# Kernel tuning notes

Measured on AMD Instinct MI355X. Metric: run time of the kernel, lower is better.

## Reference

```python
import jax, jax.numpy as jnp
import numpy as np

N_START, N_TO, E, H = 100000, 50000, 1000000, 128

def setup_inputs() -> dict:
    key = jax.random.key(0)
    ks = jax.random.split(key, 8)
    return {
        "z_start": jax.random.normal(ks[0], (N_START, H), dtype=jnp.float32),
        "z_to": jax.random.normal(ks[1], (N_TO, H), dtype=jnp.float32),
        "row": jax.random.randint(ks[2], (E,), 0, N_START, dtype=jnp.int64),
        "col": jax.random.randint(ks[3], (E,), 0, N_TO, dtype=jnp.int64),
        "W1": jax.random.normal(ks[4], (2 * H, H), dtype=jnp.float32) * (1.0 / np.sqrt(2 * H)),
        "b1": jnp.zeros((H,), dtype=jnp.float32),
        "W2": jax.random.normal(ks[5], (H, 1), dtype=jnp.float32) * (1.0 / np.sqrt(H)),
        "b2": jnp.zeros((1,), dtype=jnp.float32),
    }

def reference(z_start, z_to, row, col, W1, b1, W2, b2):
    # gather node embeddings by edge endpoints, concat along feature dim
    z = jnp.concatenate([z_start[row], z_to[col]], axis=-1)  # [E, 2H]
    h = jax.nn.relu(z @ W1 + b1)                              # [E, H]
    out = h @ W2 + b2                                         # [E, 1]
    return out.reshape(-1)
```

## Files before the change

kernel.cpp:

```cpp
#include <hip/hip_runtime.h>
#include <hip/hip_bf16.h>
#include <stdint.h>

typedef unsigned short u16;
typedef unsigned long long u64;
typedef __attribute__((ext_vector_type(8))) short short8;
typedef __attribute__((ext_vector_type(4))) float float4v;
typedef __attribute__((ext_vector_type(2))) _Float16 v2h;

__device__ __forceinline__ u16 f2bf(float x) {
    union { float f; unsigned int u; } v; v.f = x;
    unsigned int r = v.u + 0x7fffu + ((v.u >> 16) & 1u);
    return (u16)(r >> 16);
}

__device__ __forceinline__ v2h mk2h(unsigned int u) {
    union { unsigned int u; v2h h; } c; c.u = u; return c.h;
}

__device__ __forceinline__ float dot2acc(v2h a, v2h b, float s) {
#if __has_builtin(__builtin_amdgcn_fdot2)
    return __builtin_amdgcn_fdot2(a, b, s, false);
#else
    return fmaf((float)a[0], (float)b[0], fmaf((float)a[1], (float)b[1], s));
#endif
}


__global__ __launch_bounds__(256) void w1_pack(
    const float* __restrict__ W1, u16* __restrict__ w1p, int* __restrict__ cursor)
{
    if (blockIdx.x == 0 && threadIdx.x < 8) cursor[threadIdx.x] = 0;
    int w = blockIdx.x * 256 + threadIdx.x;
    int lanep = w & 63, t = (w >> 6) & 7, kc = w >> 9;
    short8 o;
#pragma unroll
    for (int j = 0; j < 8; ++j) {
        int k = kc * 32 + (lanep >> 4) * 8 + j;
        int n = t * 16 + (lanep & 15);
        o[j] = (short)f2bf(W1[k * 128 + n]);
    }
    *(short8*)(w1p + (size_t)w * 8) = o;
}

__global__ __launch_bounds__(256, 3) void uv_gemm(
    const float* __restrict__ zs, const float* __restrict__ zt,
    const u16* __restrict__ w1p, const float* __restrict__ b1,
    char* __restrict__ U8, char* __restrict__ V8,
    float* __restrict__ su, float* __restrict__ sv,
    int M1, int M2, int nU)
{
    const int tid = threadIdx.x, wave = tid >> 6, lane = tid & 63;
    const int m15 = lane & 15, quad = lane >> 4;
    const bool isV = (int)blockIdx.x >= nU;
    const float* zsrc = isV ? zt : zs;
    char* dst = isV ? V8 : U8;
    float* sdst = isV ? sv : su;
    const int row0 = (isV ? ((int)blockIdx.x - nU) : (int)blockIdx.x) * 128;
    const int M = isV ? M2 : M1;
    const int nrows = (M - row0) < 128 ? (M - row0) : 128;
    const char* wsrc = (const char*)(w1p + (isV ? 16384 : 0));

    float4 afl[2][4][2];
#pragma unroll
    for (int mtl = 0; mtl < 2; ++mtl) {
        int r = wave * 32 + mtl * 16 + m15;
        int rr = r < nrows ? r : (nrows - 1);
        const float* rowp = zsrc + (size_t)(row0 + rr) * 128 + quad * 8;
#pragma unroll
        for (int kc = 0; kc < 4; ++kc) {
            afl[mtl][kc][0] = *(const float4*)(rowp + kc * 32);
            afl[mtl][kc][1] = *(const float4*)(rowp + kc * 32 + 4);
        }
    }
    short8 Af[2][4];
#pragma unroll
    for (int mtl = 0; mtl < 2; ++mtl)
#pragma unroll
        for (int kc = 0; kc < 4; ++kc) {
            float4 x = afl[mtl][kc][0], y = afl[mtl][kc][1];
            short8 o;
            o[0] = (short)f2bf(x.x); o[1] = (short)f2bf(x.y);
            o[2] = (short)f2bf(x.z); o[3] = (short)f2bf(x.w);
            o[4] = (short)f2bf(y.x); o[5] = (short)f2bf(y.y);
            o[6] = (short)f2bf(y.z); o[7] = (short)f2bf(y.w);
            Af[mtl][kc] = o;
        }

    float4v acc[2][8];
#pragma unroll
    for (int a = 0; a < 2; ++a)
#pragma unroll
        for (int b = 0; b < 8; ++b)
            acc[a][b] = (float4v){0.f, 0.f, 0.f, 0.f};

#pragma unroll
    for (int kc = 0; kc < 4; ++kc) {
        short8 Bf[8];
#pragma unroll
        for (int t = 0; t < 8; ++t)
            Bf[t] = *(const short8*)(wsrc + ((kc * 8 + t) * 1024 + lane * 16));
#pragma unroll
        for (int t = 0; t < 8; ++t)
#pragma unroll
            for (int mtl = 0; mtl < 2; ++mtl)
                acc[mtl][t] = __builtin_amdgcn_mfma_f32_16x16x32_bf16(
                    Af[mtl][kc], Bf[t], acc[mtl][t], 0, 0, 0);
    }

    float b1v[8];
#pragma unroll
    for (int t = 0; t < 8; ++t) b1v[t] = isV ? 0.f : b1[t * 16 + m15];

#pragma unroll
    for (int mtl = 0; mtl < 2; ++mtl) {
#pragma unroll
        for (int r = 0; r < 4; ++r) {
            const int rr = wave * 32 + mtl * 16 + quad * 4 + r;
            float vals[8];
            float vmax = 0.f;
#pragma unroll
            for (int t = 0; t < 8; ++t) {
                float x = acc[mtl][t][r] + b1v[t];
                vals[t] = x;
                vmax = fmaxf(vmax, fabsf(x));
            }
            vmax = fmaxf(vmax, __shfl_xor(vmax, 1));
            vmax = fmaxf(vmax, __shfl_xor(vmax, 2));
            vmax = fmaxf(vmax, __shfl_xor(vmax, 4));
            vmax = fmaxf(vmax, __shfl_xor(vmax, 8));
            const float scl = vmax * (1.f / 127.f);
            const float rs = vmax > 0.f ? 127.f / vmax : 0.f;
            if (rr < nrows) {
                if (m15 == 0) sdst[row0 + rr] = scl;
                unsigned wlo = 0, whi = 0;
#pragma unroll
                for (int t = 0; t < 4; ++t) {
                    int q = __float2int_rn(vals[t] * rs);
                    q = q > 127 ? 127 : (q < -127 ? -127 : q);
                    wlo |= ((unsigned)q & 255u) << (8 * t);
                }
#pragma unroll
                for (int t = 4; t < 8; ++t) {
                    int q = __float2int_rn(vals[t] * rs);
                    q = q > 127 ? 127 : (q < -127 ? -127 : q);
                    whi |= ((unsigned)q & 255u) << (8 * (t - 4));
                }
                uint2 pk; pk.x = wlo; pk.y = whi;
                *(uint2*)(dst + (size_t)(row0 + rr) * 128 + m15 * 8) = pk;
            }
        }
    }
}

__global__ __launch_bounds__(256) void edge_bin(
    const int* __restrict__ row, const int* __restrict__ col,
    u64* __restrict__ tup, int* __restrict__ cursor,
    int E, float binv, int C,
    const char* __restrict__ U8, const char* __restrict__ V8,
    const float* __restrict__ su, const float* __restrict__ sv,
    const float* __restrict__ W2, const float* __restrict__ b2,
    float* __restrict__ out)
{
    __shared__ int lcnt[8];
    __shared__ int lbase[8];
    const int tid = threadIdx.x;
    if (tid < 8) lcnt[tid] = 0;
    __syncthreads();
    const int eb = blockIdx.x * 4096;
    int rr[16], cc[16], bb[16], rk[16];
#pragma unroll
    for (int it = 0; it < 16; ++it) {
        int e = eb + it * 256 + tid;
        rk[it] = -1;
        if (e < E) {
            int r = row[e], c = col[e];
            int b = (int)((float)r * binv);
            b = b > 7 ? 7 : b;
            rr[it] = r; cc[it] = c; bb[it] = b;
            rk[it] = atomicAdd(&lcnt[b], 1);
        }
    }
    __syncthreads();
    if (tid < 8) lbase[tid] = atomicAdd(&cursor[tid], lcnt[tid]);
    __syncthreads();
#pragma unroll
    for (int it = 0; it < 16; ++it) {
        if (rk[it] < 0) continue;
        int e = eb + it * 256 + tid;
        int slot = lbase[bb[it]] + rk[it];
        if (slot < C) {
            tup[(size_t)bb[it] * C + slot] =
                (u64)(unsigned)rr[it] | ((u64)(unsigned)cc[it] << 17) | ((u64)(unsigned)e << 34);
        } else {
            float a = su[rr[it]], bs = sv[cc[it]];
            const signed char* up = (const signed char*)(U8 + (size_t)rr[it] * 128);
            const signed char* vp = (const signed char*)(V8 + (size_t)cc[it] * 128);
            float s = 0.f;
            for (int p = 0; p < 128; ++p) {
                float h = fmaf(a, (float)up[p], bs * (float)vp[p]);
                h = fmaxf(h, 0.f);
                s = fmaf(h, W2[((p & 7) << 4) + (p >> 3)], s);
            }
            out[e] = s + b2[0];
        }
    }
}

__global__ __launch_bounds__(256) void edge_out(
    const char* __restrict__ U8, const char* __restrict__ V8,
    const float* __restrict__ su, const float* __restrict__ sv,
    const u64* __restrict__ tup, const int* __restrict__ cursor,
    const float* __restrict__ W2, const float* __restrict__ b2,
    float* __restrict__ out, int C, int chunks_per_bin)
{
    const int tid = threadIdx.x, m7 = tid & 7, g = tid >> 3;
    const int bin = (int)blockIdx.x & 7;
    int chunk = (int)blockIdx.x >> 3;
    int cnt = cursor[bin];
    cnt = cnt < C ? cnt : C;

    v2h w2e[4], w2o[4];
#pragma unroll
    for (int w = 0; w < 4; ++w) {
        int c0 = 2 * m7 + (w >> 1);
        int tb = (w & 1) * 4;
        w2e[w] = (v2h){(_Float16)W2[(tb + 0) * 16 + c0], (_Float16)W2[(tb + 2) * 16 + c0]};
        w2o[w] = (v2h){(_Float16)W2[(tb + 1) * 16 + c0], (_Float16)W2[(tb + 3) * 16 + c0]};
    }
    const float b2v = b2[0];
    const v2h zero2 = (v2h){(_Float16)0.f, (_Float16)0.f};
    const _Float16 mh = (_Float16)(-1152.f);
    const v2h m1152 = (v2h){mh, mh};
    const u64* tb8 = tup + (size_t)bin * C;

    for (; chunk * 256 < cnt; chunk += chunks_per_bin) {
        const int base = chunk * 256;

        u64 t[8];
#pragma unroll
        for (int it = 0; it < 8; ++it) {
            int idx = base + it * 32 + g;
            t[it] = tb8[idx < cnt ? idx : cnt - 1];
        }
        __builtin_amdgcn_sched_barrier(0);

        uint4 qu[8], qv[8];
        float fsu[8], fsv[8];
#pragma unroll
        for (int it = 0; it < 8; ++it) {
            int r = (int)(t[it] & 0x1FFFF);
            int c = (int)((t[it] >> 17) & 0x1FFFF);
            qu[it] = *(const uint4*)(U8 + (size_t)(unsigned)r * 128 + m7 * 16);
            qv[it] = *(const uint4*)(V8 + (size_t)(unsigned)c * 128 + m7 * 16);
            fsu[it] = su[r];
            fsv[it] = sv[c];
        }
        __builtin_amdgcn_sched_barrier(0);

#pragma unroll
        for (int it = 0; it < 8; ++it) {
            const float a = fsu[it], b = fsv[it];
            const _Float16 ah = (_Float16)a, bh = (_Float16)b;
            const v2h a2 = (v2h){ah, ah}, bb2 = (v2h){bh, bh};
            const unsigned int* uw = (const unsigned int*)&qu[it];
            const unsigned int* vw = (const unsigned int*)&qv[it];
            float s = 0.f;
#pragma unroll
            for (int w = 0; w < 4; ++w) {
                unsigned int xu = uw[w] ^ 0x80808080u;
                unsigned int xv = vw[w] ^ 0x80808080u;
                v2h due = mk2h((xu & 0x00FF00FFu) | 0x64006400u) + m1152;
                v2h duo = mk2h(((xu >> 8) & 0x00FF00FFu) | 0x64006400u) + m1152;
                v2h dve = mk2h((xv & 0x00FF00FFu) | 0x64006400u) + m1152;
                v2h dvo = mk2h(((xv >> 8) & 0x00FF00FFu) | 0x64006400u) + m1152;
                v2h he = __builtin_elementwise_fma(a2, due, bb2 * dve);
                he = __builtin_elementwise_max(he, zero2);
                s = dot2acc(he, w2e[w], s);
                v2h ho = __builtin_elementwise_fma(a2, duo, bb2 * dvo);
                ho = __builtin_elementwise_max(ho, zero2);
                s = dot2acc(ho, w2o[w], s);
            }
            s += __shfl_xor(s, 1);
            s += __shfl_xor(s, 2);
            s += __shfl_xor(s, 4);
            int idx = base + it * 32 + g;
            if (m7 == 0 && idx < cnt) out[(int)(t[it] >> 34)] = s + b2v;
        }
    }
}

__global__ __launch_bounds__(256) void edge_mlp_naive(
    const float* __restrict__ zs, const float* __restrict__ zt,
    const int* __restrict__ row, const int* __restrict__ col,
    const float* __restrict__ W1, const float* __restrict__ b1,
    const float* __restrict__ W2, const float* __restrict__ b2,
    float* __restrict__ out, int E)
{
    __shared__ float zr[4][256];
    int wave = threadIdx.x >> 6, lane = threadIdx.x & 63;
    int e = blockIdx.x * 4 + wave;
    int ec = e < E ? e : E - 1;
    const float* a = zs + (size_t)row[ec] * 128;
    const float* bb = zt + (size_t)col[ec] * 128;
    zr[wave][lane] = a[lane];
    zr[wave][64 + lane] = a[64 + lane];
    zr[wave][128 + lane] = bb[lane];
    zr[wave][192 + lane] = bb[64 + lane];
    __syncthreads();
    float h0 = b1[lane], h1 = b1[64 + lane];
    for (int k = 0; k < 256; ++k) {
        float zk = zr[wave][k];
        h0 = fmaf(zk, W1[k * 128 + lane], h0);
        h1 = fmaf(zk, W1[k * 128 + 64 + lane], h1);
    }
    h0 = h0 > 0.f ? h0 : 0.f;
    h1 = h1 > 0.f ? h1 : 0.f;
    float s = fmaf(h0, W2[lane], h1 * W2[64 + lane]);
    for (int m = 1; m < 64; m <<= 1) s += __shfl_xor(s, m);
    if (lane == 0 && e < E) out[e] = s + b2[0];
}

extern "C" void kernel_launch(void* const* d_in, const int* in_sizes, int n_in,
                              void* d_out, int out_size, void* d_ws, size_t ws_size,
                              hipStream_t stream) {
    const float* zs = (const float*)d_in[0];
    const float* zt = (const float*)d_in[1];
    const int*  row = (const int*)d_in[2];
    const int*  col = (const int*)d_in[3];
    const float* W1 = (const float*)d_in[4];
    const float* b1 = (const float*)d_in[5];
    const float* W2 = (const float*)d_in[6];
    const float* b2 = (const float*)d_in[7];
    float* out = (float*)d_out;

    const int nzs = in_sizes[0];
    const int nzt = in_sizes[1];
    const int E   = in_sizes[2];
    const int M1  = nzs / 128;
    const int M2  = nzt / 128;

    int C = 65536;
    while (C < E / 4 + 1024) C <<= 1;

    const size_t tup_b = (size_t)8 * C * 8;
    const size_t need = tup_b + 64 + (size_t)M1 * 4 + (size_t)M2 * 4 + 65536
                      + (size_t)nzs + (size_t)nzt;
    const bool shapes_ok = (M1 <= 131072) && (M2 <= 131072) && (E > 0) && (E < (1 << 30));

    if (!shapes_ok || ws_size < need) {
        int nb = (E + 3) / 4;
        edge_mlp_naive<<<nb, 256, 0, stream>>>(zs, zt, row, col, W1, b1, W2, b2, out, E);
        return;
    }

    u64* tup    = (u64*)d_ws;
    int* cursor = (int*)((char*)d_ws + tup_b);
    float* su   = (float*)((char*)cursor + 64);
    float* sv   = su + M1;
    u16* w1p    = (u16*)(sv + M2);
    char* U8    = (char*)(w1p + 32768);
    char* V8    = U8 + (size_t)nzs;

    w1_pack<<<16, 256, 0, stream>>>(W1, w1p, cursor);

    const int nU = (M1 + 127) / 128;
    const int nV = (M2 + 127) / 128;
    uv_gemm<<<nU + nV, 256, 0, stream>>>(zs, zt, w1p, b1, U8, V8, su, sv, M1, M2, nU);

    const int rpb = (M1 + 7) / 8;
    const float binv = 1.0f / (float)rpb;
    edge_bin<<<(E + 4095) / 4096, 256, 0, stream>>>(
        row, col, tup, cursor, E, binv, C, U8, V8, su, sv, W2, b2, out);

    const int cpb = 512;
    edge_out<<<8 * cpb, 256, 0, stream>>>(U8, V8, su, sv, tup, cursor, W2, b2, out, C, cpb);
}
```

Baseline: 179.7 us.

## Merge GEMM and edge binning into one launch, prefetch tuples, use perm decode

The U/V GEMM and edge-binning kernels become one launch whose blocks split by index, so the two phases can overlap and one kernel launch goes away. Because binning no longer waits for the GEMM, the overflow fallback recomputes the full MLP directly from fp32 inputs instead of reading the quantized U/V. The int8 storage switches to an offset-binary uint8 encoding, so edge_out can decode with a single byte-permute against a 0x64 constant instead of XOR, mask and OR. edge_out also returns early for empty chunks and software-prefetches the next chunk's edge tuples while the current one is being computed, which costs extra registers.

```diff
diff --git a/kernel.cpp b/kernel.cpp
--- a/kernel.cpp
+++ b/kernel.cpp
@@ -3,6 +3,7 @@
 #include <stdint.h>
 
 typedef unsigned short u16;
+typedef unsigned char u8;
 typedef unsigned long long u64;
 typedef __attribute__((ext_vector_type(8))) short short8;
 typedef __attribute__((ext_vector_type(4))) float float4v;
@@ -23,6 +24,21 @@
     return __builtin_amdgcn_fdot2(a, b, s, false);
 #else
     return fmaf((float)a[0], (float)b[0], fmaf((float)a[1], (float)b[1], s));
+#endif
+}
+
+__device__ __forceinline__ unsigned perm_even(unsigned x, unsigned k64) {
+#if __has_builtin(__builtin_amdgcn_perm)
+    return __builtin_amdgcn_perm(x, k64, 0x00060004u);
+#else
+    return (x & 0x00FF00FFu) | 0x64006400u;
+#endif
+}
+__device__ __forceinline__ unsigned perm_odd(unsigned x, unsigned k64) {
+#if __has_builtin(__builtin_amdgcn_perm)
+    return __builtin_amdgcn_perm(x, k64, 0x00070005u);
+#else
+    return ((x >> 8) & 0x00FF00FFu) | 0x64006400u;
 #endif
 }
 
@@ -43,172 +59,171 @@
     *(short8*)(w1p + (size_t)w * 8) = o;
 }
 
-__global__ __launch_bounds__(256, 3) void uv_gemm(
+__global__ __launch_bounds__(256, 3) void gemm_bin(
     const float* __restrict__ zs, const float* __restrict__ zt,
     const u16* __restrict__ w1p, const float* __restrict__ b1,
-    char* __restrict__ U8, char* __restrict__ V8,
+    u8* __restrict__ U8, u8* __restrict__ V8,
     float* __restrict__ su, float* __restrict__ sv,
-    int M1, int M2, int nU)
-{
-    const int tid = threadIdx.x, wave = tid >> 6, lane = tid & 63;
-    const int m15 = lane & 15, quad = lane >> 4;
-    const bool isV = (int)blockIdx.x >= nU;
-    const float* zsrc = isV ? zt : zs;
-    char* dst = isV ? V8 : U8;
-    float* sdst = isV ? sv : su;
-    const int row0 = (isV ? ((int)blockIdx.x - nU) : (int)blockIdx.x) * 128;
-    const int M = isV ? M2 : M1;
-    const int nrows = (M - row0) < 128 ? (M - row0) : 128;
-    const char* wsrc = (const char*)(w1p + (isV ? 16384 : 0));
-
-    float4 afl[2][4][2];
-#pragma unroll
-    for (int mtl = 0; mtl < 2; ++mtl) {
-        int r = wave * 32 + mtl * 16 + m15;
-        int rr = r < nrows ? r : (nrows - 1);
-        const float* rowp = zsrc + (size_t)(row0 + rr) * 128 + quad * 8;
-#pragma unroll
-        for (int kc = 0; kc < 4; ++kc) {
-            afl[mtl][kc][0] = *(const float4*)(rowp + kc * 32);
-            afl[mtl][kc][1] = *(const float4*)(rowp + kc * 32 + 4);
-        }
-    }
-    short8 Af[2][4];
-#pragma unroll
-    for (int mtl = 0; mtl < 2; ++mtl)
-#pragma unroll
-        for (int kc = 0; kc < 4; ++kc) {
-            float4 x = afl[mtl][kc][0], y = afl[mtl][kc][1];
-            short8 o;
-            o[0] = (short)f2bf(x.x); o[1] = (short)f2bf(x.y);
-            o[2] = (short)f2bf(x.z); o[3] = (short)f2bf(x.w);
-            o[4] = (short)f2bf(y.x); o[5] = (short)f2bf(y.y);
-            o[6] = (short)f2bf(y.z); o[7] = (short)f2bf(y.w);
-            Af[mtl][kc] = o;
-        }
-
-    float4v acc[2][8];
-#pragma unroll
-    for (int a = 0; a < 2; ++a)
-#pragma unroll
-        for (int b = 0; b < 8; ++b)
-            acc[a][b] = (float4v){0.f, 0.f, 0.f, 0.f};
-
-#pragma unroll
-    for (int kc = 0; kc < 4; ++kc) {
-        short8 Bf[8];
-#pragma unroll
-        for (int t = 0; t < 8; ++t)
-            Bf[t] = *(const short8*)(wsrc + ((kc * 8 + t) * 1024 + lane * 16));
-#pragma unroll
-        for (int t = 0; t < 8; ++t)
-#pragma unroll
-            for (int mtl = 0; mtl < 2; ++mtl)
-                acc[mtl][t] = __builtin_amdgcn_mfma_f32_16x16x32_bf16(
-                    Af[mtl][kc], Bf[t], acc[mtl][t], 0, 0, 0);
-    }
-
-    float b1v[8];
-#pragma unroll
-    for (int t = 0; t < 8; ++t) b1v[t] = isV ? 0.f : b1[t * 16 + m15];
-
-#pragma unroll
-    for (int mtl = 0; mtl < 2; ++mtl) {
-#pragma unroll
-        for (int r = 0; r < 4; ++r) {
-            const int rr = wave * 32 + mtl * 16 + quad * 4 + r;
-            float vals[8];
-            float vmax = 0.f;
-#pragma unroll
-            for (int t = 0; t < 8; ++t) {
-                float x = acc[mtl][t][r] + b1v[t];
-                vals[t] = x;
-                vmax = fmaxf(vmax, fabsf(x));
-            }
-            vmax = fmaxf(vmax, __shfl_xor(vmax, 1));
-            vmax = fmaxf(vmax, __shfl_xor(vmax, 2));
-            vmax = fmaxf(vmax, __shfl_xor(vmax, 4));
-            vmax = fmaxf(vmax, __shfl_xor(vmax, 8));
-            const float scl = vmax * (1.f / 127.f);
-            const float rs = vmax > 0.f ? 127.f / vmax : 0.f;
-            if (rr < nrows) {
-                if (m15 == 0) sdst[row0 + rr] = scl;
-                unsigned wlo = 0, whi = 0;
-#pragma unroll
-                for (int t = 0; t < 4; ++t) {
-                    int q = __float2int_rn(vals[t] * rs);
-                    q = q > 127 ? 127 : (q < -127 ? -127 : q);
-                    wlo |= ((unsigned)q & 255u) << (8 * t);
-                }
-#pragma unroll
-                for (int t = 4; t < 8; ++t) {
-                    int q = __float2int_rn(vals[t] * rs);
-                    q = q > 127 ? 127 : (q < -127 ? -127 : q);
-                    whi |= ((unsigned)q & 255u) << (8 * (t - 4));
-                }
-                uint2 pk; pk.x = wlo; pk.y = whi;
-                *(uint2*)(dst + (size_t)(row0 + rr) * 128 + m15 * 8) = pk;
-            }
-        }
-    }
-}
-
-__global__ __launch_bounds__(256) void edge_bin(
+    int M1, int M2, int nU, int nGemm,
     const int* __restrict__ row, const int* __restrict__ col,
     u64* __restrict__ tup, int* __restrict__ cursor,
     int E, float binv, int C,
-    const char* __restrict__ U8, const char* __restrict__ V8,
-    const float* __restrict__ su, const float* __restrict__ sv,
-    const float* __restrict__ W2, const float* __restrict__ b2,
-    float* __restrict__ out)
+    const float* __restrict__ W1, const float* __restrict__ W2,
+    const float* __restrict__ b2, float* __restrict__ out)
 {
     __shared__ int lcnt[8];
     __shared__ int lbase[8];
-    const int tid = threadIdx.x;
-    if (tid < 8) lcnt[tid] = 0;
-    __syncthreads();
-    const int eb = blockIdx.x * 4096;
-    int rr[16], cc[16], bb[16], rk[16];
-#pragma unroll
-    for (int it = 0; it < 16; ++it) {
-        int e = eb + it * 256 + tid;
-        rk[it] = -1;
-        if (e < E) {
-            int r = row[e], c = col[e];
-            int b = (int)((float)r * binv);
-            b = b > 7 ? 7 : b;
-            rr[it] = r; cc[it] = c; bb[it] = b;
-            rk[it] = atomicAdd(&lcnt[b], 1);
-        }
-    }
-    __syncthreads();
-    if (tid < 8) lbase[tid] = atomicAdd(&cursor[tid], lcnt[tid]);
-    __syncthreads();
-#pragma unroll
-    for (int it = 0; it < 16; ++it) {
-        if (rk[it] < 0) continue;
-        int e = eb + it * 256 + tid;
-        int slot = lbase[bb[it]] + rk[it];
-        if (slot < C) {
-            tup[(size_t)bb[it] * C + slot] =
-                (u64)(unsigned)rr[it] | ((u64)(unsigned)cc[it] << 17) | ((u64)(unsigned)e << 34);
-        } else {
-            float a = su[rr[it]], bs = sv[cc[it]];
-            const signed char* up = (const signed char*)(U8 + (size_t)rr[it] * 128);
-            const signed char* vp = (const signed char*)(V8 + (size_t)cc[it] * 128);
-            float s = 0.f;
-            for (int p = 0; p < 128; ++p) {
-                float h = fmaf(a, (float)up[p], bs * (float)vp[p]);
-                h = fmaxf(h, 0.f);
-                s = fmaf(h, W2[((p & 7) << 4) + (p >> 3)], s);
-            }
-            out[e] = s + b2[0];
+
+    if ((int)blockIdx.x < nGemm) {
+        const int tid = threadIdx.x, wave = tid >> 6, lane = tid & 63;
+        const int m15 = lane & 15, quad = lane >> 4;
+        const bool isV = (int)blockIdx.x >= nU;
+        const float* zsrc = isV ? zt : zs;
+        u8* dst = isV ? V8 : U8;
+        float* sdst = isV ? sv : su;
+        const int row0 = (isV ? ((int)blockIdx.x - nU) : (int)blockIdx.x) * 128;
+        const int M = isV ? M2 : M1;
+        const int nrows = (M - row0) < 128 ? (M - row0) : 128;
+        const char* wsrc = (const char*)(w1p + (isV ? 16384 : 0));
+
+        float4 afl[2][4][2];
+#pragma unroll
+        for (int mtl = 0; mtl < 2; ++mtl) {
+            int r = wave * 32 + mtl * 16 + m15;
+            int rr = r < nrows ? r : (nrows - 1);
+            const float* rowp = zsrc + (size_t)(row0 + rr) * 128 + quad * 8;
+#pragma unroll
+            for (int kc = 0; kc < 4; ++kc) {
+                afl[mtl][kc][0] = *(const float4*)(rowp + kc * 32);
+                afl[mtl][kc][1] = *(const float4*)(rowp + kc * 32 + 4);
+            }
+        }
+        short8 Af[2][4];
+#pragma unroll
+        for (int mtl = 0; mtl < 2; ++mtl)
+#pragma unroll
+            for (int kc = 0; kc < 4; ++kc) {
+                float4 x = afl[mtl][kc][0], y = afl[mtl][kc][1];
+                short8 o;
+                o[0] = (short)f2bf(x.x); o[1] = (short)f2bf(x.y);
+                o[2] = (short)f2bf(x.z); o[3] = (short)f2bf(x.w);
+                o[4] = (short)f2bf(y.x); o[5] = (short)f2bf(y.y);
+                o[6] = (short)f2bf(y.z); o[7] = (short)f2bf(y.w);
+                Af[mtl][kc] = o;
+            }
+
+        float4v acc[2][8];
+#pragma unroll
+        for (int a = 0; a < 2; ++a)
+#pragma unroll
+            for (int b = 0; b < 8; ++b)
+                acc[a][b] = (float4v){0.f, 0.f, 0.f, 0.f};
+
+#pragma unroll
+        for (int kc = 0; kc < 4; ++kc) {
+            short8 Bf[8];
+#pragma unroll
+            for (int t = 0; t < 8; ++t)
+                Bf[t] = *(const short8*)(wsrc + ((kc * 8 + t) * 1024 + lane * 16));
+#pragma unroll
+            for (int t = 0; t < 8; ++t)
+#pragma unroll
+                for (int mtl = 0; mtl < 2; ++mtl)
+                    acc[mtl][t] = __builtin_amdgcn_mfma_f32_16x16x32_bf16(
+                        Af[mtl][kc], Bf[t], acc[mtl][t], 0, 0, 0);
+        }
+
+        float b1v[8];
+#pragma unroll
+        for (int t = 0; t < 8; ++t) b1v[t] = isV ? 0.f : b1[t * 16 + m15];
+
+#pragma unroll
+        for (int mtl = 0; mtl < 2; ++mtl) {
+#pragma unroll
+            for (int r = 0; r < 4; ++r) {
+                const int rr = wave * 32 + mtl * 16 + quad * 4 + r;
+                float vals[8];
+                float vmax = 0.f;
+#pragma unroll
+                for (int t = 0; t < 8; ++t) {
+                    float x = acc[mtl][t][r] + b1v[t];
+                    vals[t] = x;
+                    vmax = fmaxf(vmax, fabsf(x));
+                }
+                vmax = fmaxf(vmax, __shfl_xor(vmax, 1));
+                vmax = fmaxf(vmax, __shfl_xor(vmax, 2));
+                vmax = fmaxf(vmax, __shfl_xor(vmax, 4));
+                vmax = fmaxf(vmax, __shfl_xor(vmax, 8));
+                const float scl = vmax * (1.f / 127.f);
+                const float rs = vmax > 0.f ? 127.f / vmax : 0.f;
+                if (rr < nrows) {
+                    if (m15 == 0) sdst[row0 + rr] = scl;
+                    unsigned wlo = 0, whi = 0;
+#pragma unroll
+                    for (int t = 0; t < 4; ++t) {
+                        int q = __float2int_rn(vals[t] * rs);
+                        q = q > 127 ? 127 : (q < -127 ? -127 : q);
+                        wlo |= (unsigned)(q + 128) << (8 * t);
+                    }
+#pragma unroll
+                    for (int t = 4; t < 8; ++t) {
+                        int q = __float2int_rn(vals[t] * rs);
+                        q = q > 127 ? 127 : (q < -127 ? -127 : q);
+                        whi |= (unsigned)(q + 128) << (8 * (t - 4));
+                    }
+                    uint2 pk; pk.x = wlo; pk.y = whi;
+                    *(uint2*)(dst + (size_t)(row0 + rr) * 128 + m15 * 8) = pk;
+                }
+            }
+        }
+    } else {
+        const int tid = threadIdx.x;
+        if (tid < 8) lcnt[tid] = 0;
+        __syncthreads();
+        const int eb = ((int)blockIdx.x - nGemm) * 4096;
+        int rr[16], cc[16], bb[16], rk[16];
+#pragma unroll
+        for (int it = 0; it < 16; ++it) {
+            int e = eb + it * 256 + tid;
+            rk[it] = -1;
+            if (e < E) {
+                int r = row[e], c = col[e];
+                int b = (int)((float)r * binv);
+                b = b > 7 ? 7 : b;
+                rr[it] = r; cc[it] = c; bb[it] = b;
+                rk[it] = atomicAdd(&lcnt[b], 1);
+            }
+        }
+        __syncthreads();
+        if (tid < 8) lbase[tid] = atomicAdd(&cursor[tid], lcnt[tid]);
+        __syncthreads();
+#pragma unroll
+        for (int it = 0; it < 16; ++it) {
+            if (rk[it] < 0) continue;
+            int e = eb + it * 256 + tid;
+            int slot = lbase[bb[it]] + rk[it];
+            if (slot < C) {
+                tup[(size_t)bb[it] * C + slot] =
+                    (u64)(unsigned)rr[it] | ((u64)(unsigned)cc[it] << 17) | ((u64)(unsigned)e << 34);
+            } else {
+                const float* za = zs + (size_t)rr[it] * 128;
+                const float* zb = zt + (size_t)cc[it] * 128;
+                float s = 0.f;
+                for (int j = 0; j < 128; ++j) {
+                    float h = b1[j];
+                    for (int k = 0; k < 128; ++k) h = fmaf(za[k], W1[k * 128 + j], h);
+                    for (int k = 0; k < 128; ++k) h = fmaf(zb[k], W1[(128 + k) * 128 + j], h);
+                    h = fmaxf(h, 0.f);
+                    s = fmaf(h, W2[j], s);
+                }
+                out[e] = s + b2[0];
+            }
         }
     }
 }
 
 __global__ __launch_bounds__(256) void edge_out(
-    const char* __restrict__ U8, const char* __restrict__ V8,
+    const u8* __restrict__ U8, const u8* __restrict__ V8,
     const float* __restrict__ su, const float* __restrict__ sv,
     const u64* __restrict__ tup, const int* __restrict__ cursor,
     const float* __restrict__ W2, const float* __restrict__ b2,
@@ -219,6 +234,7 @@
     int chunk = (int)blockIdx.x >> 3;
     int cnt = cursor[bin];
     cnt = cnt < C ? cnt : C;
+    if (chunk * 256 >= cnt) return;
 
     v2h w2e[4], w2o[4];
 #pragma unroll
@@ -232,17 +248,18 @@
     const v2h zero2 = (v2h){(_Float16)0.f, (_Float16)0.f};
     const _Float16 mh = (_Float16)(-1152.f);
     const v2h m1152 = (v2h){mh, mh};
+    const unsigned k64 = 0x64646464u;
     const u64* tb8 = tup + (size_t)bin * C;
+
+    u64 t[8];
+#pragma unroll
+    for (int it = 0; it < 8; ++it) {
+        int idx = chunk * 256 + it * 32 + g;
+        t[it] = tb8[idx < cnt ? idx : cnt - 1];
+    }
 
     for (; chunk * 256 < cnt; chunk += chunks_per_bin) {
         const int base = chunk * 256;
-
-        u64 t[8];
-#pragma unroll
-        for (int it = 0; it < 8; ++it) {
-            int idx = base + it * 32 + g;
-            t[it] = tb8[idx < cnt ? idx : cnt - 1];
-        }
         __builtin_amdgcn_sched_barrier(0);
 
         uint4 qu[8], qv[8];
@@ -258,6 +275,18 @@
         }
         __builtin_amdgcn_sched_barrier(0);
 
+        const int nbase = (chunk + chunks_per_bin) * 256;
+        u64 tn[8];
+        const bool more = nbase < cnt;
+        if (more) {
+#pragma unroll
+            for (int it = 0; it < 8; ++it) {
+                int idx = nbase + it * 32 + g;
+                tn[it] = tb8[idx < cnt ? idx : cnt - 1];
+            }
+        }
+        __builtin_amdgcn_sched_barrier(0);
+
 #pragma unroll
         for (int it = 0; it < 8; ++it) {
             const float a = fsu[it], b = fsv[it];
@@ -268,12 +297,10 @@
             float s = 0.f;
 #pragma unroll
             for (int w = 0; w < 4; ++w) {
-                unsigned int xu = uw[w] ^ 0x80808080u;
-                unsigned int xv = vw[w] ^ 0x80808080u;
-                v2h due = mk2h((xu & 0x00FF00FFu) | 0x64006400u) + m1152;
-                v2h duo = mk2h(((xu >> 8) & 0x00FF00FFu) | 0x64006400u) + m1152;
-                v2h dve = mk2h((xv & 0x00FF00FFu) | 0x64006400u) + m1152;
-                v2h dvo = mk2h(((xv >> 8) & 0x00FF00FFu) | 0x64006400u) + m1152;
+                v2h due = mk2h(perm_even(uw[w], k64)) + m1152;
+                v2h duo = mk2h(perm_odd (uw[w], k64)) + m1152;
+                v2h dve = mk2h(perm_even(vw[w], k64)) + m1152;
+                v2h dvo = mk2h(perm_odd (vw[w], k64)) + m1152;
                 v2h he = __builtin_elementwise_fma(a2, due, bb2 * dve);
                 he = __builtin_elementwise_max(he, zero2);
                 s = dot2acc(he, w2e[w], s);
@@ -286,6 +313,10 @@
             s += __shfl_xor(s, 4);
             int idx = base + it * 32 + g;
             if (m7 == 0 && idx < cnt) out[(int)(t[it] >> 34)] = s + b2v;
+        }
+        if (more) {
+#pragma unroll
+            for (int it = 0; it < 8; ++it) t[it] = tn[it];
         }
     }
 }
@@ -359,19 +390,21 @@
     float* su   = (float*)((char*)cursor + 64);
     float* sv   = su + M1;
     u16* w1p    = (u16*)(sv + M2);
-    char* U8    = (char*)(w1p + 32768);
-    char* V8    = U8 + (size_t)nzs;
+    u8* U8      = (u8*)(w1p + 32768);
+    u8* V8      = U8 + (size_t)nzs;
 
     w1_pack<<<16, 256, 0, stream>>>(W1, w1p, cursor);
 
     const int nU = (M1 + 127) / 128;
     const int nV = (M2 + 127) / 128;
-    uv_gemm<<<nU + nV, 256, 0, stream>>>(zs, zt, w1p, b1, U8, V8, su, sv, M1, M2, nU);
-
+    const int nGemm = nU + nV;
+    const int nBin = (E + 4095) / 4096;
     const int rpb = (M1 + 7) / 8;
     const float binv = 1.0f / (float)rpb;
-    edge_bin<<<(E + 4095) / 4096, 256, 0, stream>>>(
-        row, col, tup, cursor, E, binv, C, U8, V8, su, sv, W2, b2, out);
+
+    gemm_bin<<<nGemm + nBin, 256, 0, stream>>>(
+        zs, zt, w1p, b1, U8, V8, su, sv, M1, M2, nU, nGemm,
+        row, col, tup, cursor, E, binv, C, W1, W2, b2, out);
 
     const int cpb = 512;
     edge_out<<<8 * cpb, 256, 0, stream>>>(U8, V8, su, sv, tup, cursor, W2, b2, out, C, cpb);
```

Result: faster. 171.8 us (-4.4%).
